# Kernel tuning notes

Hardware: AMD Instinct MI355X
Metric: run time of the kernel (lower is better)

Reference implementation:

```python
import jax, jax.numpy as jnp
import numpy as np

B, S, D = 4, 2048, 1024      # batch, seq, d_model
H = 4096                     # expert hidden_size
E, K = 8, 2                  # num_experts, top_k
Z_COEF, BAL_COEF = 0.001, 0.01


def setup_inputs() -> dict:
    key = jax.random.key(0)
    ks = jax.random.split(key, 10)
    sc = 0.02
    return {
        "x": jax.random.normal(ks[0], (B, S, D), jnp.float32),
        "gate_w": jax.random.normal(ks[1], (D, E), jnp.float32) * sc,
        "keys_w": jax.random.normal(ks[2], (E, D, H), jnp.float32) * sc,
        "keys_b": jnp.zeros((E, H), jnp.float32),
        "values_w": jax.random.normal(ks[3], (E, H, D), jnp.float32) * sc,
        "values_b": jnp.zeros((E, D), jnp.float32),
        "shared_keys_w": jax.random.normal(ks[4], (D, H), jnp.float32) * sc,
        "shared_keys_b": jnp.zeros((H,), jnp.float32),
        "shared_values_w": jax.random.normal(ks[5], (H, D), jnp.float32) * sc,
        "shared_values_b": jnp.zeros((D,), jnp.float32),
    }


def reference(x, gate_w, keys_w, keys_b, values_w, values_b,
              shared_keys_w, shared_keys_b, shared_values_w, shared_values_b):
    b, s, d = x.shape
    xf = x.reshape(-1, d)                                  # [N, D]

    # ---- Router (top-k, softmax over selected scores) ----
    logits = xf @ gate_w                                   # [N, E]
    scores, idx = jax.lax.top_k(logits, K)                 # [N, K]
    w = jax.nn.softmax(scores, axis=-1)                    # [N, K]

    # Aux losses (training path)
    one_hot = jax.nn.one_hot(idx, E, dtype=w.dtype)        # [N, K, E]
    usage = (one_hot * w[..., None]).sum(axis=(0, 1))      # [E]
    balance_loss = usage.std() / usage.mean() * BAL_COEF
    z_loss = jnp.square(jax.nn.logsumexp(logits, axis=-1)).mean() * Z_COEF
    router_loss = balance_loss + z_loss

    # ---- Shared expert(s): single FFN, divided by count (=1) ----
    out = jax.nn.gelu(xf @ shared_keys_w + shared_keys_b) @ shared_values_w + shared_values_b

    # ---- Training path: dense per-expert FFN, masked combine ----
    # hidden: [N, E, H]
    hidden = jax.nn.gelu(jnp.einsum('nd,edh->neh', xf, keys_w) + keys_b)
    expert_out = jnp.einsum('neh,ehd->ned', hidden, values_w) + values_b  # [N, E, D]
    comb = (one_hot * w[..., None]).sum(axis=1)            # [N, E] per-token expert weight
    out = out + jnp.einsum('ned,ne->nd', expert_out, comb)

    return out.reshape(b, s, d), router_loss
```

## Files before the change

kernel.cpp:

```cpp
#include <hip/hip_runtime.h>
#include <hip/hip_bf16.h>


#define N_TOK 8192
#define DM    1024
#define HD    4096
#define NE    8
#define NKTOT 16384
#define PERM_CAP 17408
#define MAX_TILES 136
#define BAND 17
#define RTOK_BLK 16

typedef __attribute__((ext_vector_type(8))) short bhalf8;
typedef __attribute__((ext_vector_type(4))) float floatx4;

__device__ __forceinline__ unsigned short f2bf(float f) {
  union { float f; unsigned int u; } v; v.f = f;
  unsigned int u = v.u;
  return (unsigned short)((u + 0x7fffu + ((u >> 16) & 1u)) >> 16);
}

__device__ __forceinline__ float bf2f(unsigned short h) {
  union { unsigned int u; float f; } v; v.u = ((unsigned int)h) << 16;
  return v.f;
}

__device__ __forceinline__ float gelu_tanh(float h) {
  float u = 0.7978845608028654f * (h + 0.044715f * h * h * h);
  float t = 1.0f - 2.0f / (1.0f + __expf(2.0f * u));
  return 0.5f * h * (1.0f + t);
}

__device__ __forceinline__ void gload16(const unsigned short* g, void* l) {
  __builtin_amdgcn_global_load_lds(
      (const __attribute__((address_space(1))) void*)g,
      (__attribute__((address_space(3))) void*)l, 16, 0, 0);
}

__global__ void init_kernel(int* perm, float* permw, float* usage, float* zsum,
                            int* counts, int* fill) {
  int i = blockIdx.x * 256 + threadIdx.x;
  if (i < PERM_CAP) { perm[i] = 0; permw[i] = 0.0f; }
  if (i < NE) { usage[i] = 0.0f; counts[i] = 0; fill[i] = 0; }
  if (i == 0) zsum[0] = 0.0f;
}

__global__ void cvt_x_kernel(const float* __restrict__ x, unsigned short* __restrict__ xb) {
  size_t i = (size_t)(blockIdx.x * 256 + threadIdx.x) * 4;
  float4 v = *(const float4*)(x + i);
  ushort4 o;
  o.x = f2bf(v.x); o.y = f2bf(v.y); o.z = f2bf(v.z); o.w = f2bf(v.w);
  *(ushort4*)(xb + i) = o;
}

__global__ void router_kernel(const float* __restrict__ x, const float* __restrict__ gw,
                              int* __restrict__ idxb, float* __restrict__ wbuf,
                              float* __restrict__ usage, float* __restrict__ zsum,
                              int* __restrict__ counts) {
  __shared__ float s_use[NE];
  __shared__ int   s_cnt[NE];
  __shared__ float s_z;
  int t = threadIdx.x;
  if (t < NE) { s_use[t] = 0.0f; s_cnt[t] = 0; }
  if (t == 0) s_z = 0.0f;
  __syncthreads();

  int wave = t >> 6;
  int lane = t & 63;

  float luse[NE]; int lcnt[NE];
#pragma unroll
  for (int e = 0; e < NE; e++) { luse[e] = 0.0f; lcnt[e] = 0; }
  float lz = 0.0f;

#pragma unroll
  for (int i = 0; i < 4; i++) {
    int n = blockIdx.x * RTOK_BLK + wave * 4 + i;
    const float* xr = x + (size_t)n * DM;
    float acc[NE];
#pragma unroll
    for (int e = 0; e < NE; e++) acc[e] = 0.0f;
    for (int d = lane; d < DM; d += 64) {
      float xv = xr[d];
      const float* g = gw + (size_t)d * NE;
#pragma unroll
      for (int e = 0; e < NE; e++) acc[e] += xv * g[e];
    }
#pragma unroll
    for (int e = 0; e < NE; e++) {
#pragma unroll
      for (int off = 32; off > 0; off >>= 1) acc[e] += __shfl_xor(acc[e], off);
    }
    if (lane == 0) {
      float m1 = acc[0]; int i1 = 0;
#pragma unroll
      for (int e = 1; e < NE; e++) if (acc[e] > m1) { m1 = acc[e]; i1 = e; }
      float m2 = -3.0e38f; int i2 = 0;
#pragma unroll
      for (int e = 0; e < NE; e++) if (e != i1 && acc[e] > m2) { m2 = acc[e]; i2 = e; }
      float e1 = __expf(m2 - m1);
      float w1 = 1.0f / (1.0f + e1);
      float w2 = e1 / (1.0f + e1);
      float s = 0.0f;
#pragma unroll
      for (int e = 0; e < NE; e++) s += __expf(acc[e] - m1);
      float lse = m1 + __logf(s);
      idxb[n * 2 + 0] = i1; idxb[n * 2 + 1] = i2;
      wbuf[n * 2 + 0] = w1; wbuf[n * 2 + 1] = w2;
      luse[i1] += w1; luse[i2] += w2;
      lcnt[i1]++;     lcnt[i2]++;
      lz += lse * lse;
    }
  }

  if (lane == 0) {
#pragma unroll
    for (int e = 0; e < NE; e++) {
      atomicAdd(&s_use[e], luse[e]);
      atomicAdd(&s_cnt[e], lcnt[e]);
    }
    atomicAdd(&s_z, lz);
  }
  __syncthreads();
  if (t < NE) {
    atomicAdd(&usage[t], s_use[t]);
    atomicAdd(&counts[t], s_cnt[t]);
  }
  if (t == 0) atomicAdd(zsum, s_z);
}

__global__ void scan_kernel(const int* __restrict__ counts, int* __restrict__ poff,
                            int* __restrict__ tileE, int* __restrict__ tileR,
                            int* __restrict__ nTiles,
                            const float* __restrict__ usage, const float* __restrict__ zsum,
                            float* __restrict__ lossOut) {
  if (threadIdx.x == 0 && blockIdx.x == 0) {
    int run = 0, nt = 0;
    for (int e = 0; e < NE; e++) {
      poff[e] = run;
      int t = (counts[e] + 127) >> 7;
      for (int i = 0; i < t; i++) { tileE[nt] = e; tileR[nt] = run + i * 128; nt++; }
      run += t << 7;
    }
    *nTiles = nt;
    float mean = 0.0f;
    for (int e = 0; e < NE; e++) mean += usage[e];
    mean *= (1.0f / NE);
    float var = 0.0f;
    for (int e = 0; e < NE; e++) { float d = usage[e] - mean; var += d * d; }
    var *= (1.0f / NE);
    float bal = sqrtf(var) / mean * 0.01f;
    float z = (zsum[0] / (float)N_TOK) * 0.001f;
    lossOut[0] = bal + z;
  }
}

__global__ void scatter_kernel(const int* __restrict__ idxb, const float* __restrict__ wbuf,
                               const int* __restrict__ poff, int* __restrict__ fill,
                               int* __restrict__ perm, float* __restrict__ permw,
                               int* __restrict__ pos) {
  __shared__ int lcnt[NE];
  __shared__ int lbase[NE];
  int t = threadIdx.x;
  if (t < NE) lcnt[t] = 0;
  __syncthreads();
  int i = blockIdx.x * 256 + t;
  int e = idxb[i];
  int r = atomicAdd(&lcnt[e], 1);
  __syncthreads();
  if (t < NE) lbase[t] = atomicAdd(&fill[t], lcnt[t]);
  __syncthreads();
  int p = poff[e] + lbase[e] + r;
  perm[p] = i >> 1;
  permw[p] = wbuf[i];
  pos[i] = p;
}

__global__ void transpose_cvt_kernel(const float* __restrict__ src,
                                     unsigned short* __restrict__ dst, int R, int C) {
  __shared__ float tile[64][65];
  size_t bo = (size_t)blockIdx.z * R * C;
  src += bo; dst += bo;
  int r0 = blockIdx.x * 64, c0 = blockIdx.y * 64;
  int c = threadIdx.x & 63, r = threadIdx.x >> 6;
#pragma unroll
  for (int i = 0; i < 16; i++)
    tile[r + i * 4][c] = src[(size_t)(r0 + r + i * 4) * C + c0 + c];
  __syncthreads();
#pragma unroll
  for (int i = 0; i < 16; i++) {
    int oc = r + i * 4;
    float v = tile[c][oc];
    dst[(size_t)(c0 + oc) * R + r0 + c] = f2bf(v);
  }
}

__global__ void combine_kernel(float* __restrict__ out,
                               const unsigned short* __restrict__ eout,
                               const int* __restrict__ pos) {
  int t = blockIdx.x;
  int d = threadIdx.x * 8;
  int p0 = pos[t * 2], p1 = pos[t * 2 + 1];
  float* o = out + (size_t)t * DM + d;
  const unsigned short* e0 = eout + (size_t)p0 * DM + d;
  const unsigned short* e1 = eout + (size_t)p1 * DM + d;
  float4 a = *(const float4*)(o);
  float4 b = *(const float4*)(o + 4);
  ushort4 u0a = *(const ushort4*)(e0), u0b = *(const ushort4*)(e0 + 4);
  ushort4 u1a = *(const ushort4*)(e1), u1b = *(const ushort4*)(e1 + 4);
  a.x += bf2f(u0a.x) + bf2f(u1a.x);
  a.y += bf2f(u0a.y) + bf2f(u1a.y);
  a.z += bf2f(u0a.z) + bf2f(u1a.z);
  a.w += bf2f(u0a.w) + bf2f(u1a.w);
  b.x += bf2f(u0b.x) + bf2f(u1b.x);
  b.y += bf2f(u0b.y) + bf2f(u1b.y);
  b.z += bf2f(u0b.z) + bf2f(u1b.z);
  b.w += bf2f(u0b.w) + bf2f(u1b.w);
  *(float4*)(o) = a;
  *(float4*)(o + 4) = b;
}

template<int MODE>
__device__ __forceinline__ void gemm_body(
    const unsigned short* __restrict__ A,
    const unsigned short* __restrict__ BT,
    const float* __restrict__ bias,
    float* __restrict__ outF,
    unsigned short* __restrict__ outH,
    int Kd, int Nd,
    const int* __restrict__ perm,
    const float* __restrict__ permw,
    const int* __restrict__ tileE,
    const int* __restrict__ tileR,
    const int* __restrict__ nTiles) {
  __shared__ unsigned short As[2 * 128 * 64];
  __shared__ unsigned short Bs[2 * 128 * 64];

  int id = blockIdx.x;
  int xcd = id & 7, q = id >> 3;
  int mt, ntile;
  if (MODE == 0) {
    mt = xcd * 8 + (q & 7);
    ntile = q >> 3;
  } else if (MODE == 1) {
    ntile = q & 7;
    mt = xcd * 8 + (q >> 3);
  } else if (MODE == 2) {
    int n_in = q & 7, m_in = (q >> 3) & 3, ng = (q >> 5) & 3, mg = q >> 7;
    int mband = mg * 4 + m_in;
    if (mband >= BAND) return;
    mt = xcd * BAND + mband;
    ntile = ng * 8 + n_in;
  } else {
    mt = xcd * BAND + (q >> 3);
    ntile = q & 7;
  }

  int n0 = ntile * 128;
  int prow0 = 0, m0 = 0;
  if (MODE >= 2) {
    if (mt >= *nTiles) return;
    int e = tileE[mt];
    prow0 = tileR[mt];
    BT += (size_t)e * Kd * Nd;
    bias += (size_t)e * Nd;
  } else {
    m0 = mt * 128;
  }

  int t = threadIdx.x;
  int rsub = t >> 3;
  int gc = (t & 7) ^ (rsub & 7);
  const unsigned short* aptr[4];
  const unsigned short* bptr[4];
#pragma unroll
  for (int p = 0; p < 4; p++) {
    int r = rsub + p * 32;
    size_t grow;
    if (MODE == 2)      grow = (size_t)perm[prow0 + r];
    else if (MODE == 3) grow = (size_t)(prow0 + r);
    else                grow = (size_t)(m0 + r);
    aptr[p] = A + grow * Kd + gc * 8;
    bptr[p] = BT + (size_t)(n0 + r) * Kd + gc * 8;
  }
  char* ldsA = (char*)As + (t & 192) * 16;
  char* ldsB = (char*)Bs + (t & 192) * 16;

  int lane = t & 63;
  int wv = t >> 6;
  int wm = (wv >> 1) * 64, wn = (wv & 1) * 64;
  int lr = lane & 15, lq = lane >> 4;
  int rx = lr & 7;

  floatx4 acc[4][4];
#pragma unroll
  for (int i = 0; i < 4; i++)
#pragma unroll
    for (int j = 0; j < 4; j++) acc[i][j] = (floatx4){0.f, 0.f, 0.f, 0.f};

#pragma unroll
  for (int p = 0; p < 4; p++) {
    gload16(aptr[p], ldsA + p * 4096);
    gload16(bptr[p], ldsB + p * 4096);
  }
  __syncthreads();

  int buf = 0;
  for (int k0 = 0; k0 < Kd; k0 += 64) {
    int nk = k0 + 64;
    if (nk < Kd) {
      char* la = ldsA + (buf ^ 1) * 16384;
      char* lb = ldsB + (buf ^ 1) * 16384;
#pragma unroll
      for (int p = 0; p < 4; p++) {
        gload16(aptr[p] + nk, la + p * 4096);
        gload16(bptr[p] + nk, lb + p * 4096);
      }
    }
    const unsigned short* Ab = As + buf * 8192;
    const unsigned short* Bb = Bs + buf * 8192;
#pragma unroll
    for (int kk = 0; kk < 2; kk++) {
      int ca = kk * 4 + lq;
      bhalf8 af[4], bf[4];
#pragma unroll
      for (int i = 0; i < 4; i++) {
        af[i] = *(const bhalf8*)&Ab[(wm + i * 16 + lr) * 64 + (ca ^ rx) * 8];
        bf[i] = *(const bhalf8*)&Bb[(wn + i * 16 + lr) * 64 + (ca ^ rx) * 8];
      }
#pragma unroll
      for (int mtile = 0; mtile < 4; mtile++)
#pragma unroll
        for (int ntl = 0; ntl < 4; ntl++)
          acc[mtile][ntl] = __builtin_amdgcn_mfma_f32_16x16x32_bf16(af[mtile], bf[ntl], acc[mtile][ntl], 0, 0, 0);
    }
    __syncthreads();
    buf ^= 1;
  }

#pragma unroll
  for (int mtile = 0; mtile < 4; mtile++) {
#pragma unroll
    for (int ntl = 0; ntl < 4; ntl++) {
      int ncol = n0 + wn + ntl * 16 + lr;
      float bb = bias[ncol];
#pragma unroll
      for (int r = 0; r < 4; r++) {
        int mrow = wm + mtile * 16 + lq * 4 + r;
        float v = acc[mtile][ntl][r] + bb;
        if (MODE == 0) {
          outH[(size_t)(m0 + mrow) * Nd + ncol] = f2bf(gelu_tanh(v));
        } else if (MODE == 1) {
          outF[(size_t)(m0 + mrow) * Nd + ncol] = v;
        } else if (MODE == 2) {
          outH[(size_t)(prow0 + mrow) * Nd + ncol] = f2bf(gelu_tanh(v));
        } else {
          int prow = prow0 + mrow;
          float w = permw[prow];
          outH[(size_t)prow * Nd + ncol] = f2bf(w * v);
        }
      }
    }
  }
}

__global__ __launch_bounds__(256) void gemm_shared_keys(
    const unsigned short* A, const unsigned short* BT, const float* bias,
    float* outF, unsigned short* outH, int Kd, int Nd,
    const int* perm, const float* permw, const int* tE, const int* tR, const int* nT) {
  gemm_body<0>(A, BT, bias, outF, outH, Kd, Nd, perm, permw, tE, tR, nT);
}
__global__ __launch_bounds__(256) void gemm_shared_values(
    const unsigned short* A, const unsigned short* BT, const float* bias,
    float* outF, unsigned short* outH, int Kd, int Nd,
    const int* perm, const float* permw, const int* tE, const int* tR, const int* nT) {
  gemm_body<1>(A, BT, bias, outF, outH, Kd, Nd, perm, permw, tE, tR, nT);
}
__global__ __launch_bounds__(256) void gemm_expert_keys(
    const unsigned short* A, const unsigned short* BT, const float* bias,
    float* outF, unsigned short* outH, int Kd, int Nd,
    const int* perm, const float* permw, const int* tE, const int* tR, const int* nT) {
  gemm_body<2>(A, BT, bias, outF, outH, Kd, Nd, perm, permw, tE, tR, nT);
}
__global__ __launch_bounds__(256) void gemm_expert_values(
    const unsigned short* A, const unsigned short* BT, const float* bias,
    float* outF, unsigned short* outH, int Kd, int Nd,
    const int* perm, const float* permw, const int* tE, const int* tR, const int* nT) {
  gemm_body<3>(A, BT, bias, outF, outH, Kd, Nd, perm, permw, tE, tR, nT);
}

extern "C" void kernel_launch(void* const* d_in, const int* in_sizes, int n_in,
                              void* d_out, int out_size, void* d_ws, size_t ws_size,
                              hipStream_t stream) {
  const float* x        = (const float*)d_in[0];
  const float* gate_w   = (const float*)d_in[1];
  const float* keys_w   = (const float*)d_in[2];
  const float* keys_b   = (const float*)d_in[3];
  const float* values_w = (const float*)d_in[4];
  const float* values_b = (const float*)d_in[5];
  const float* sk_w     = (const float*)d_in[6];
  const float* sk_b     = (const float*)d_in[7];
  const float* sv_w     = (const float*)d_in[8];
  const float* sv_b     = (const float*)d_in[9];
  float* out = (float*)d_out;

  char* p = (char*)d_ws;
  unsigned short* xb   = (unsigned short*)p; p += (size_t)N_TOK * DM * 2;
  unsigned short* wt   = (unsigned short*)p; p += (size_t)NE * DM * HD * 2;
  unsigned short* hid  = (unsigned short*)p; p += (size_t)PERM_CAP * HD * 2;
  unsigned short* eout = (unsigned short*)p; p += (size_t)PERM_CAP * DM * 2;
  int*   idxb   = (int*)p;   p += NKTOT * 4;
  float* wbuf   = (float*)p; p += NKTOT * 4;
  int*   perm   = (int*)p;   p += PERM_CAP * 4;
  float* permw  = (float*)p; p += PERM_CAP * 4;
  int*   pos    = (int*)p;   p += NKTOT * 4;
  int*   counts = (int*)p;   p += NE * 4;
  int*   fill   = (int*)p;   p += NE * 4;
  int*   poff   = (int*)p;   p += NE * 4;
  float* usage  = (float*)p; p += NE * 4;
  float* zsum   = (float*)p; p += 16;
  int*   tileE  = (int*)p;   p += MAX_TILES * 4;
  int*   tileR  = (int*)p;   p += MAX_TILES * 4;
  int*   nTiles = (int*)p;   p += 16;

  float* lossOut = out + (size_t)N_TOK * DM;

  init_kernel<<<(PERM_CAP + 255) / 256, 256, 0, stream>>>(perm, permw, usage, zsum, counts, fill);
  cvt_x_kernel<<<(N_TOK * DM / 4 + 255) / 256, 256, 0, stream>>>(x, xb);
  router_kernel<<<N_TOK / RTOK_BLK, 256, 0, stream>>>(x, gate_w, idxb, wbuf, usage, zsum, counts);
  scan_kernel<<<1, 64, 0, stream>>>(counts, poff, tileE, tileR, nTiles, usage, zsum, lossOut);
  scatter_kernel<<<NKTOT / 256, 256, 0, stream>>>(idxb, wbuf, poff, fill, perm, permw, pos);

  transpose_cvt_kernel<<<dim3(DM / 64, HD / 64, 1), 256, 0, stream>>>(sk_w, wt, DM, HD);
  gemm_shared_keys<<<2048, 256, 0, stream>>>(
      xb, wt, sk_b, nullptr, hid, DM, HD, perm, permw, tileE, tileR, nTiles);
  transpose_cvt_kernel<<<dim3(HD / 64, DM / 64, 1), 256, 0, stream>>>(sv_w, wt, HD, DM);
  gemm_shared_values<<<512, 256, 0, stream>>>(
      hid, wt, sv_b, out, nullptr, HD, DM, perm, permw, tileE, tileR, nTiles);

  transpose_cvt_kernel<<<dim3(DM / 64, HD / 64, NE), 256, 0, stream>>>(keys_w, wt, DM, HD);
  gemm_expert_keys<<<5120, 256, 0, stream>>>(
      xb, wt, keys_b, nullptr, hid, DM, HD, perm, permw, tileE, tileR, nTiles);
  transpose_cvt_kernel<<<dim3(HD / 64, DM / 64, NE), 256, 0, stream>>>(values_w, wt, HD, DM);
  gemm_expert_values<<<1088, 256, 0, stream>>>(
      hid, wt, values_b, nullptr, eout, HD, DM, perm, permw, tileE, tileR, nTiles);

  combine_kernel<<<N_TOK, 128, 0, stream>>>(out, eout, pos);
}
```

Measured before the change: 1.044 ms.

## Enlarge GEMM tiles to 256x256 with 8 waves and ping-pong staged pipeline

Replaces the 128x128, 4-wave GEMM with 256x256 tiles computed by 512 threads (8 waves, each owning 128x64). The K loop is split into four MFMA phases interleaved with partial global-to-LDS stages, explicit vmcnt/lgkmcnt waits, raw s_barriers and setprio, so loads overlap compute. Expert routing padding moves from 128 to 256 rows, and grid sizes and launch bounds change to match. This raises arithmetic intensity and cuts LDS and global traffic per FLOP, in exchange for more padding waste in the expert GEMMs, fewer blocks (possible tail imbalance on the small shared-values GEMM), and reliance on hand-placed wait counts being correct.

Result: slower. 1.113 ms (+6.6%).

```diff
diff --git a/kernel.cpp b/kernel.cpp
--- a/kernel.cpp
+++ b/kernel.cpp
@@ -7,13 +7,15 @@
 #define HD    4096
 #define NE    8
 #define NKTOT 16384
-#define PERM_CAP 17408
-#define MAX_TILES 136
-#define BAND 17
+#define PERM_CAP 18432
+#define MAX_TILES 72
 #define RTOK_BLK 16
 
 typedef __attribute__((ext_vector_type(8))) short bhalf8;
 typedef __attribute__((ext_vector_type(4))) float floatx4;
+
+#define MEMBAR asm volatile("" ::: "memory")
+#define SBAR   do { MEMBAR; __builtin_amdgcn_s_barrier(); MEMBAR; } while (0)
 
 __device__ __forceinline__ unsigned short f2bf(float f) {
   union { float f; unsigned int u; } v; v.f = f;
@@ -139,9 +141,9 @@
     int run = 0, nt = 0;
     for (int e = 0; e < NE; e++) {
       poff[e] = run;
-      int t = (counts[e] + 127) >> 7;
-      for (int i = 0; i < t; i++) { tileE[nt] = e; tileR[nt] = run + i * 128; nt++; }
-      run += t << 7;
+      int t = (counts[e] + 255) >> 8;
+      for (int i = 0; i < t; i++) { tileE[nt] = e; tileR[nt] = run + i * 256; nt++; }
+      run += t << 8;
     }
     *nTiles = nt;
     float mean = 0.0f;
@@ -234,30 +236,18 @@
     const int* __restrict__ tileE,
     const int* __restrict__ tileR,
     const int* __restrict__ nTiles) {
-  __shared__ unsigned short As[2 * 128 * 64];
-  __shared__ unsigned short Bs[2 * 128 * 64];
+  __shared__ __align__(16) unsigned short As[2][16384];
+  __shared__ __align__(16) unsigned short Bs[2][16384];
 
   int id = blockIdx.x;
   int xcd = id & 7, q = id >> 3;
   int mt, ntile;
-  if (MODE == 0) {
-    mt = xcd * 8 + (q & 7);
-    ntile = q >> 3;
-  } else if (MODE == 1) {
-    ntile = q & 7;
-    mt = xcd * 8 + (q >> 3);
-  } else if (MODE == 2) {
-    int n_in = q & 7, m_in = (q >> 3) & 3, ng = (q >> 5) & 3, mg = q >> 7;
-    int mband = mg * 4 + m_in;
-    if (mband >= BAND) return;
-    mt = xcd * BAND + mband;
-    ntile = ng * 8 + n_in;
-  } else {
-    mt = xcd * BAND + (q >> 3);
-    ntile = q & 7;
-  }
-
-  int n0 = ntile * 128;
+  if (MODE == 0)      { mt = xcd * 4 + (q & 3); ntile = q >> 2; }
+  else if (MODE == 1) { mt = xcd * 4 + (q & 3); ntile = q >> 2; }
+  else if (MODE == 2) { mt = xcd * 9 + (q >> 4); ntile = q & 15; }
+  else                { mt = xcd * 9 + (q >> 2); ntile = q & 3; }
+
+  int n0 = ntile * 256;
   int prow0 = 0, m0 = 0;
   if (MODE >= 2) {
     if (mt >= *nTiles) return;
@@ -266,89 +256,155 @@
     BT += (size_t)e * Kd * Nd;
     bias += (size_t)e * Nd;
   } else {
-    m0 = mt * 128;
+    m0 = mt * 256;
   }
 
   int t = threadIdx.x;
+  int wid = t >> 6, lane = t & 63;
   int rsub = t >> 3;
-  int gc = (t & 7) ^ (rsub & 7);
+  int cc = (t & 7) ^ (rsub & 7);
   const unsigned short* aptr[4];
   const unsigned short* bptr[4];
 #pragma unroll
-  for (int p = 0; p < 4; p++) {
-    int r = rsub + p * 32;
+  for (int c = 0; c < 4; c++) {
+    int r = c * 64 + rsub;
     size_t grow;
     if (MODE == 2)      grow = (size_t)perm[prow0 + r];
     else if (MODE == 3) grow = (size_t)(prow0 + r);
     else                grow = (size_t)(m0 + r);
-    aptr[p] = A + grow * Kd + gc * 8;
-    bptr[p] = BT + (size_t)(n0 + r) * Kd + gc * 8;
-  }
-  char* ldsA = (char*)As + (t & 192) * 16;
-  char* ldsB = (char*)Bs + (t & 192) * 16;
-
-  int lane = t & 63;
-  int wv = t >> 6;
-  int wm = (wv >> 1) * 64, wn = (wv & 1) * 64;
+    aptr[c] = A + grow * Kd + cc * 8;
+    bptr[c] = BT + (size_t)(n0 + r) * Kd + cc * 8;
+  }
+  char* aS = (char*)&As[0][0] + wid * 1024;
+  char* bS = (char*)&Bs[0][0] + wid * 1024;
+
+#define STAGE_A(kt, h, slot) do { \
+    gload16(aptr[(h)*2]     + (kt)*64, aS + (slot)*32768 + (h)*16384); \
+    gload16(aptr[(h)*2 + 1] + (kt)*64, aS + (slot)*32768 + (h)*16384 + 8192); } while (0)
+#define STAGE_B(kt, h, slot) do { \
+    gload16(bptr[(h)*2]     + (kt)*64, bS + (slot)*32768 + (h)*16384); \
+    gload16(bptr[(h)*2 + 1] + (kt)*64, bS + (slot)*32768 + (h)*16384 + 8192); } while (0)
+
+  int wr = wid >> 2, wc = wid & 3;
   int lr = lane & 15, lq = lane >> 4;
   int rx = lr & 7;
-
-  floatx4 acc[4][4];
-#pragma unroll
-  for (int i = 0; i < 4; i++)
+  int aoff = (wr * 128 + lr) * 64;
+  int boff = (wc * 64 + lr) * 64;
+  int c0 = (lq ^ rx) * 8;
+
+  floatx4 acc[8][4];
+#pragma unroll
+  for (int i = 0; i < 8; i++)
 #pragma unroll
     for (int j = 0; j < 4; j++) acc[i][j] = (floatx4){0.f, 0.f, 0.f, 0.f};
 
-#pragma unroll
-  for (int p = 0; p < 4; p++) {
-    gload16(aptr[p], ldsA + p * 4096);
-    gload16(bptr[p], ldsB + p * 4096);
-  }
-  __syncthreads();
-
-  int buf = 0;
-  for (int k0 = 0; k0 < Kd; k0 += 64) {
-    int nk = k0 + 64;
-    if (nk < Kd) {
-      char* la = ldsA + (buf ^ 1) * 16384;
-      char* lb = ldsB + (buf ^ 1) * 16384;
-#pragma unroll
-      for (int p = 0; p < 4; p++) {
-        gload16(aptr[p] + nk, la + p * 4096);
-        gload16(bptr[p] + nk, lb + p * 4096);
-      }
-    }
-    const unsigned short* Ab = As + buf * 8192;
-    const unsigned short* Bb = Bs + buf * 8192;
-#pragma unroll
-    for (int kk = 0; kk < 2; kk++) {
-      int ca = kk * 4 + lq;
-      bhalf8 af[4], bf[4];
-#pragma unroll
-      for (int i = 0; i < 4; i++) {
-        af[i] = *(const bhalf8*)&Ab[(wm + i * 16 + lr) * 64 + (ca ^ rx) * 8];
-        bf[i] = *(const bhalf8*)&Bb[(wn + i * 16 + lr) * 64 + (ca ^ rx) * 8];
-      }
-#pragma unroll
-      for (int mtile = 0; mtile < 4; mtile++)
-#pragma unroll
-        for (int ntl = 0; ntl < 4; ntl++)
-          acc[mtile][ntl] = __builtin_amdgcn_mfma_f32_16x16x32_bf16(af[mtile], bf[ntl], acc[mtile][ntl], 0, 0, 0);
-    }
-    __syncthreads();
-    buf ^= 1;
-  }
-
-#pragma unroll
-  for (int mtile = 0; mtile < 4; mtile++) {
-#pragma unroll
-    for (int ntl = 0; ntl < 4; ntl++) {
-      int ncol = n0 + wn + ntl * 16 + lr;
-      float bb = bias[ncol];
+  int nkt = Kd >> 6;
+
+  STAGE_A(0, 0, 0); STAGE_A(0, 1, 0);
+  STAGE_B(0, 0, 0); STAGE_B(0, 1, 0);
+  STAGE_B(1, 0, 1); STAGE_B(1, 1, 1);
+  asm volatile("s_waitcnt vmcnt(4)" ::: "memory");
+  SBAR;
+
+  bhalf8 a[4][2], bL[2][2], bH[2][2];
+  for (int kt = 0; kt < nkt; ++kt) {
+    int s = kt & 1;
+    const unsigned short* Ax = &As[0][0] + s * 16384;
+    const unsigned short* Bx = &Bs[0][0] + s * 16384;
+
+#pragma unroll
+    for (int i = 0; i < 4; i++) {
+      a[i][0] = *(const bhalf8*)&Ax[aoff + i * 1024 + c0];
+      a[i][1] = *(const bhalf8*)&Ax[aoff + i * 1024 + (c0 ^ 32)];
+    }
+#pragma unroll
+    for (int j = 0; j < 2; j++) {
+      bL[j][0] = *(const bhalf8*)&Bx[boff + j * 1024 + c0];
+      bL[j][1] = *(const bhalf8*)&Bx[boff + j * 1024 + (c0 ^ 32)];
+    }
+    if (kt + 1 < nkt) STAGE_A(kt + 1, 0, s ^ 1);
+    SBAR;
+    asm volatile("s_waitcnt lgkmcnt(0)" ::: "memory");
+    __builtin_amdgcn_s_setprio(1);
+#pragma unroll
+    for (int kk = 0; kk < 2; kk++)
+#pragma unroll
+      for (int i = 0; i < 4; i++)
+#pragma unroll
+        for (int j = 0; j < 2; j++)
+          acc[i][j] = __builtin_amdgcn_mfma_f32_16x16x32_bf16(a[i][kk], bL[j][kk], acc[i][j], 0, 0, 0);
+    __builtin_amdgcn_s_setprio(0);
+    SBAR;
+
+#pragma unroll
+    for (int j = 0; j < 2; j++) {
+      bH[j][0] = *(const bhalf8*)&Bx[boff + (j + 2) * 1024 + c0];
+      bH[j][1] = *(const bhalf8*)&Bx[boff + (j + 2) * 1024 + (c0 ^ 32)];
+    }
+    if (kt + 1 < nkt) STAGE_A(kt + 1, 1, s ^ 1);
+    SBAR;
+    asm volatile("s_waitcnt lgkmcnt(0)" ::: "memory");
+    __builtin_amdgcn_s_setprio(1);
+#pragma unroll
+    for (int kk = 0; kk < 2; kk++)
+#pragma unroll
+      for (int i = 0; i < 4; i++)
+#pragma unroll
+        for (int j = 0; j < 2; j++)
+          acc[i][j + 2] = __builtin_amdgcn_mfma_f32_16x16x32_bf16(a[i][kk], bH[j][kk], acc[i][j + 2], 0, 0, 0);
+    __builtin_amdgcn_s_setprio(0);
+    SBAR;
+
+#pragma unroll
+    for (int i = 0; i < 4; i++) {
+      a[i][0] = *(const bhalf8*)&Ax[aoff + (i + 4) * 1024 + c0];
+      a[i][1] = *(const bhalf8*)&Ax[aoff + (i + 4) * 1024 + (c0 ^ 32)];
+    }
+    if (kt + 2 < nkt) STAGE_B(kt + 2, 0, s);
+    SBAR;
+    asm volatile("s_waitcnt lgkmcnt(0)" ::: "memory");
+    __builtin_amdgcn_s_setprio(1);
+#pragma unroll
+    for (int kk = 0; kk < 2; kk++)
+#pragma unroll
+      for (int i = 0; i < 4; i++)
+#pragma unroll
+        for (int j = 0; j < 2; j++)
+          acc[i + 4][j] = __builtin_amdgcn_mfma_f32_16x16x32_bf16(a[i][kk], bL[j][kk], acc[i + 4][j], 0, 0, 0);
+    __builtin_amdgcn_s_setprio(0);
+    SBAR;
+
+    if (kt + 2 < nkt) {
+      STAGE_B(kt + 2, 1, s);
+      asm volatile("s_waitcnt vmcnt(4)" ::: "memory");
+    } else {
+      asm volatile("s_waitcnt vmcnt(0)" ::: "memory");
+    }
+    SBAR;
+    __builtin_amdgcn_s_setprio(1);
+#pragma unroll
+    for (int kk = 0; kk < 2; kk++)
+#pragma unroll
+      for (int i = 0; i < 4; i++)
+#pragma unroll
+        for (int j = 0; j < 2; j++)
+          acc[i + 4][j + 2] = __builtin_amdgcn_mfma_f32_16x16x32_bf16(a[i][kk], bH[j][kk], acc[i + 4][j + 2], 0, 0, 0);
+    __builtin_amdgcn_s_setprio(0);
+    SBAR;
+  }
+#undef STAGE_A
+#undef STAGE_B
+
+#pragma unroll
+  for (int jj = 0; jj < 4; jj++) {
+    int ncol = n0 + wc * 64 + jj * 16 + lr;
+    float bb = bias[ncol];
+#pragma unroll
+    for (int i = 0; i < 8; i++) {
 #pragma unroll
       for (int r = 0; r < 4; r++) {
-        int mrow = wm + mtile * 16 + lq * 4 + r;
-        float v = acc[mtile][ntl][r] + bb;
+        int mrow = wr * 128 + i * 16 + lq * 4 + r;
+        float v = acc[i][jj][r] + bb;
         if (MODE == 0) {
           outH[(size_t)(m0 + mrow) * Nd + ncol] = f2bf(gelu_tanh(v));
         } else if (MODE == 1) {
@@ -365,25 +421,25 @@
   }
 }
 
-__global__ __launch_bounds__(256) void gemm_shared_keys(
+__global__ __launch_bounds__(512, 2) void gemm_shared_keys(
     const unsigned short* A, const unsigned short* BT, const float* bias,
     float* outF, unsigned short* outH, int Kd, int Nd,
     const int* perm, const float* permw, const int* tE, const int* tR, const int* nT) {
   gemm_body<0>(A, BT, bias, outF, outH, Kd, Nd, perm, permw, tE, tR, nT);
 }
-__global__ __launch_bounds__(256) void gemm_shared_values(
+__global__ __launch_bounds__(512, 2) void gemm_shared_values(
     const unsigned short* A, const unsigned short* BT, const float* bias,
     float* outF, unsigned short* outH, int Kd, int Nd,
     const int* perm, const float* permw, const int* tE, const int* tR, const int* nT) {
   gemm_body<1>(A, BT, bias, outF, outH, Kd, Nd, perm, permw, tE, tR, nT);
 }
-__global__ __launch_bounds__(256) void gemm_expert_keys(
+__global__ __launch_bounds__(512, 2) void gemm_expert_keys(
     const unsigned short* A, const unsigned short* BT, const float* bias,
     float* outF, unsigned short* outH, int Kd, int Nd,
     const int* perm, const float* permw, const int* tE, const int* tR, const int* nT) {
   gemm_body<2>(A, BT, bias, outF, outH, Kd, Nd, perm, permw, tE, tR, nT);
 }
-__global__ __launch_bounds__(256) void gemm_expert_values(
+__global__ __launch_bounds__(512, 2) void gemm_expert_values(
     const unsigned short* A, const unsigned short* BT, const float* bias,
     float* outF, unsigned short* outH, int Kd, int Nd,
     const int* perm, const float* permw, const int* tE, const int* tR, const int* nT) {
@@ -433,17 +489,17 @@
   scatter_kernel<<<NKTOT / 256, 256, 0, stream>>>(idxb, wbuf, poff, fill, perm, permw, pos);
 
   transpose_cvt_kernel<<<dim3(DM / 64, HD / 64, 1), 256, 0, stream>>>(sk_w, wt, DM, HD);
-  gemm_shared_keys<<<2048, 256, 0, stream>>>(
+  gemm_shared_keys<<<512, 512, 0, stream>>>(
       xb, wt, sk_b, nullptr, hid, DM, HD, perm, permw, tileE, tileR, nTiles);
   transpose_cvt_kernel<<<dim3(HD / 64, DM / 64, 1), 256, 0, stream>>>(sv_w, wt, HD, DM);
-  gemm_shared_values<<<512, 256, 0, stream>>>(
+  gemm_shared_values<<<128, 512, 0, stream>>>(
       hid, wt, sv_b, out, nullptr, HD, DM, perm, permw, tileE, tileR, nTiles);
 
   transpose_cvt_kernel<<<dim3(DM / 64, HD / 64, NE), 256, 0, stream>>>(keys_w, wt, DM, HD);
-  gemm_expert_keys<<<5120, 256, 0, stream>>>(
+  gemm_expert_keys<<<1152, 512, 0, stream>>>(
       xb, wt, keys_b, nullptr, hid, DM, HD, perm, permw, tileE, tileR, nTiles);
   transpose_cvt_kernel<<<dim3(HD / 64, DM / 64, NE), 256, 0, stream>>>(values_w, wt, HD, DM);
-  gemm_expert_values<<<1088, 256, 0, stream>>>(
+  gemm_expert_values<<<288, 512, 0, stream>>>(
       hid, wt, values_b, nullptr, eout, HD, DM, perm, permw, tileE, tileR, nTiles);
 
   combine_kernel<<<N_TOK, 128, 0, stream>>>(out, eout, pos);
```

## Replace LDS double buffering with single buffer and raise occupancy hint

Applied to the files above, without the earlier changes.

Removes the double-buffered LDS prefetch pipeline from the shared GEMM body, cutting LDS per block from 64KB to 32KB, and loads each K tile synchronously before computing. It also adds a min-blocks-per-CU hint of 4 to all four GEMM kernels, so more workgroups can be resident and hide latency through occupancy instead of software pipelining. The cost is that global-to-LDS loads no longer overlap MFMA work within a block, and the launch bound may force register spilling with the 64 float accumulators per thread.

Result: faster. 926.4 us (-11.2%).

```diff
diff --git a/kernel.cpp b/kernel.cpp
--- a/kernel.cpp
+++ b/kernel.cpp
@@ -234,8 +234,8 @@
     const int* __restrict__ tileE,
     const int* __restrict__ tileR,
     const int* __restrict__ nTiles) {
-  __shared__ unsigned short As[2 * 128 * 64];
-  __shared__ unsigned short Bs[2 * 128 * 64];
+  __shared__ __align__(16) unsigned short As[128 * 64];
+  __shared__ __align__(16) unsigned short Bs[128 * 64];
 
   int id = blockIdx.x;
   int xcd = id & 7, q = id >> 3;
@@ -299,35 +299,21 @@
 #pragma unroll
     for (int j = 0; j < 4; j++) acc[i][j] = (floatx4){0.f, 0.f, 0.f, 0.f};
 
-#pragma unroll
-  for (int p = 0; p < 4; p++) {
-    gload16(aptr[p], ldsA + p * 4096);
-    gload16(bptr[p], ldsB + p * 4096);
-  }
-  __syncthreads();
-
-  int buf = 0;
   for (int k0 = 0; k0 < Kd; k0 += 64) {
-    int nk = k0 + 64;
-    if (nk < Kd) {
-      char* la = ldsA + (buf ^ 1) * 16384;
-      char* lb = ldsB + (buf ^ 1) * 16384;
-#pragma unroll
-      for (int p = 0; p < 4; p++) {
-        gload16(aptr[p] + nk, la + p * 4096);
-        gload16(bptr[p] + nk, lb + p * 4096);
-      }
-    }
-    const unsigned short* Ab = As + buf * 8192;
-    const unsigned short* Bb = Bs + buf * 8192;
+#pragma unroll
+    for (int p = 0; p < 4; p++) {
+      gload16(aptr[p] + k0, ldsA + p * 4096);
+      gload16(bptr[p] + k0, ldsB + p * 4096);
+    }
+    __syncthreads();
 #pragma unroll
     for (int kk = 0; kk < 2; kk++) {
       int ca = kk * 4 + lq;
       bhalf8 af[4], bf[4];
 #pragma unroll
       for (int i = 0; i < 4; i++) {
-        af[i] = *(const bhalf8*)&Ab[(wm + i * 16 + lr) * 64 + (ca ^ rx) * 8];
-        bf[i] = *(const bhalf8*)&Bb[(wn + i * 16 + lr) * 64 + (ca ^ rx) * 8];
+        af[i] = *(const bhalf8*)&As[(wm + i * 16 + lr) * 64 + ((ca ^ rx) * 8)];
+        bf[i] = *(const bhalf8*)&Bs[(wn + i * 16 + lr) * 64 + ((ca ^ rx) * 8)];
       }
 #pragma unroll
       for (int mtile = 0; mtile < 4; mtile++)
@@ -336,7 +322,6 @@
           acc[mtile][ntl] = __builtin_amdgcn_mfma_f32_16x16x32_bf16(af[mtile], bf[ntl], acc[mtile][ntl], 0, 0, 0);
     }
     __syncthreads();
-    buf ^= 1;
   }
 
 #pragma unroll
@@ -365,25 +350,25 @@
   }
 }
 
-__global__ __launch_bounds__(256) void gemm_shared_keys(
+__global__ __launch_bounds__(256, 4) void gemm_shared_keys(
     const unsigned short* A, const unsigned short* BT, const float* bias,
     float* outF, unsigned short* outH, int Kd, int Nd,
     const int* perm, const float* permw, const int* tE, const int* tR, const int* nT) {
   gemm_body<0>(A, BT, bias, outF, outH, Kd, Nd, perm, permw, tE, tR, nT);
 }
-__global__ __launch_bounds__(256) void gemm_shared_values(
+__global__ __launch_bounds__(256, 4) void gemm_shared_values(
     const unsigned short* A, const unsigned short* BT, const float* bias,
     float* outF, unsigned short* outH, int Kd, int Nd,
     const int* perm, const float* permw, const int* tE, const int* tR, const int* nT) {
   gemm_body<1>(A, BT, bias, outF, outH, Kd, Nd, perm, permw, tE, tR, nT);
 }
-__global__ __launch_bounds__(256) void gemm_expert_keys(
+__global__ __launch_bounds__(256, 4) void gemm_expert_keys(
     const unsigned short* A, const unsigned short* BT, const float* bias,
     float* outF, unsigned short* outH, int Kd, int Nd,
     const int* perm, const float* permw, const int* tE, const int* tR, const int* nT) {
   gemm_body<2>(A, BT, bias, outF, outH, Kd, Nd, perm, permw, tE, tR, nT);
 }
-__global__ __launch_bounds__(256) void gemm_expert_values(
+__global__ __launch_bounds__(256, 4) void gemm_expert_values(
     const unsigned short* A, const unsigned short* BT, const float* bias,
     float* outF, unsigned short* outH, int Kd, int Nd,
     const int* perm, const float* permw, const int* tE, const int* tR, const int* nT) {
```
